# Kernel tuning notes

Measured on AMD Instinct MI355X. Metric: run time of the kernel, lower is better.

## Reference

```python
import jax, jax.numpy as jnp
import numpy as np

F_DIM = 256
N_HEADS = 4
D_Q = F_DIM // N_HEADS  # 64
EPS = 1e-6


def layer_norm(x, g, b):
    mu = jnp.mean(x, axis=-1, keepdims=True)
    var = jnp.mean(jnp.square(x - mu), axis=-1, keepdims=True)
    return (x - mu) * jax.lax.rsqrt(var + EPS) * g + b


def linear(x, W, b):
    # torch nn.Linear: y = x @ W.T + b, W: [out, in]
    return jnp.einsum('...i,oi->...o', x, W) + b


def setup_inputs() -> dict:
    key = jax.random.key(0)
    ks = jax.random.split(key, 16)
    f = F_DIM
    inp = {
        'code_map': jax.random.normal(ks[0], (8, 512, f), jnp.float32),
        'texture_map': jax.random.normal(ks[1], (8, 512, f), jnp.float32),
        'Wq': jax.random.normal(ks[2], (N_HEADS * D_Q, f), jnp.float32) * 0.02,
        'bq': jnp.zeros((N_HEADS * D_Q,), jnp.float32),
        'Wk': jax.random.normal(ks[3], (N_HEADS * D_Q, f), jnp.float32) * 0.02,
        'bk': jnp.zeros((N_HEADS * D_Q,), jnp.float32),
        'Wv': jax.random.normal(ks[4], (N_HEADS * D_Q, f), jnp.float32) * 0.02,
        'bv': jnp.zeros((N_HEADS * D_Q,), jnp.float32),
        'Wo': jax.random.normal(ks[5], (f, N_HEADS * D_Q), jnp.float32) * 0.02,
        'bo': jnp.zeros((f,), jnp.float32),
        'ln1_g': jnp.ones((f,), jnp.float32), 'ln1_b': jnp.zeros((f,), jnp.float32),
        'ln2_g': jnp.ones((f,), jnp.float32), 'ln2_b': jnp.zeros((f,), jnp.float32),
        'ffln_g': jnp.ones((f,), jnp.float32), 'ffln_b': jnp.zeros((f,), jnp.float32),
        'W1': jax.random.normal(ks[6], (f, f), jnp.float32) * 0.02,
        'b1': jnp.zeros((f,), jnp.float32),
        'W2': jax.random.normal(ks[7], (f, f), jnp.float32) * 0.02,
        'b2': jnp.zeros((f,), jnp.float32),
    }
    return inp


def reference(code_map, texture_map, Wq, bq, Wk, bk, Wv, bv, Wo, bo,
              ln1_g, ln1_b, ln2_g, ln2_b, ffln_g, ffln_b, W1, b1, W2, b2):
    n_code, V, f = code_map.shape
    bs = texture_map.shape[0]
    h, dq = N_HEADS, D_Q

    # LayerNorms (code side -> ln1, texture side -> ln2); expansion via repeat
    # is a pure broadcast, so keep code side [n_code,...] and texture side [bs,...].
    code2 = layer_norm(code_map, ln1_g, ln1_b)       # [n, V, f]
    tex2 = layer_norm(texture_map, ln2_g, ln2_b)     # [b, V, f]

    q = linear(tex2, Wq, bq).reshape(bs, V, h, dq)    # [b, V, h, d]
    k = linear(code2, Wk, bk).reshape(n_code, V, h, dq)
    v = linear(code2, Wv, bv).reshape(n_code, V, h, dq)

    scale = 1.0 / jnp.sqrt(jnp.asarray(dq, q.dtype))
    # scores: [b, n, h, Vq, Vk]
    scores = jnp.einsum('bqhd,nkhd->bnhqk', q, k) * scale
    attn = jax.nn.softmax(scores, axis=-1)
    ctx = jnp.einsum('bnhqk,nkhd->bnhqd', attn, v)    # [b, n, h, V, d]
    ctx = ctx.transpose(0, 1, 3, 2, 4).reshape(bs, n_code, V, h * dq)
    feat = linear(ctx, Wo, bo)                        # [b, n, V, f]

    x = texture_map[:, None, :, :] + feat             # residual with broadcast
    # ffR: MLP_res_block
    y = layer_norm(x, ffln_g, ffln_b)
    y = linear(jax.nn.relu(linear(y, W1, b1)), W2, b2)
    return x + y
```

## Files before the change

### kernel.cpp

```cpp
#include <hip/hip_runtime.h>
#include <hip/hip_bf16.h>

#define F 256
#define V 512
#define NB 8
#define NC 8
#define NH 4
#define DQ 64
#define EPS 1e-6f

typedef __hip_bfloat16 bf16;
typedef __attribute__((ext_vector_type(8))) short short8;
typedef __attribute__((ext_vector_type(4))) float f32x4;
typedef __attribute__((ext_vector_type(4))) unsigned uint4v;

__device__ __forceinline__ float b2f(bf16 x){ return __bfloat162float(x); }
__device__ __forceinline__ float shf(short s){
    return __bfloat162float(__builtin_bit_cast(bf16, (unsigned short)s));
}

#define MFMA(a,b,c) __builtin_amdgcn_mfma_f32_16x16x32_bf16((a),(b),(c),0,0,0)

__device__ __forceinline__ unsigned pack2bf(float a, float b){
    unsigned short ua = __builtin_bit_cast(unsigned short, __float2bfloat16(a));
    unsigned short ub = __builtin_bit_cast(unsigned short, __float2bfloat16(b));
    return (unsigned)ua | ((unsigned)ub << 16);
}

__global__ __launch_bounds__(256) void pre_kernel(const float* __restrict__ code,
                          const float* __restrict__ tex,
                          const float* __restrict__ ln1_g, const float* __restrict__ ln1_b,
                          const float* __restrict__ ln2_g, const float* __restrict__ ln2_b,
                          const float* __restrict__ w0, const float* __restrict__ w1,
                          const float* __restrict__ w2, const float* __restrict__ w3,
                          const float* __restrict__ w4, const float* __restrict__ w5,
                          bf16* __restrict__ cn, bf16* __restrict__ tn, bf16* __restrict__ tb,
                          bf16* __restrict__ wdst){
    if (blockIdx.x >= 2048){
        int bid = blockIdx.x - 2048;
        int which = bid >> 6;
        int idx = (((bid & 63) << 8) | threadIdx.x) << 2;
        const float* s = which==0?w0: which==1?w1: which==2?w2: which==3?w3: which==4?w4: w5;
        float4 v = *(const float4*)(s + idx);
        uint2 p; p.x = pack2bf(v.x, v.y); p.y = pack2bf(v.z, v.w);
        *(uint2*)(wdst + which * (F*F) + idx) = p;
        return;
    }
    int w = threadIdx.x >> 6, lane = threadIdx.x & 63;
    int r = blockIdx.x * 4 + w;
    int is_tex = r >> 12;
    int row = r & 4095;
    const float* src = is_tex ? tex : code;
    const float* g   = is_tex ? ln2_g : ln1_g;
    const float* be  = is_tex ? ln2_b : ln1_b;
    bf16* dst        = is_tex ? tn : cn;

    float4 x = *(const float4*)(src + row * F + lane * 4);
    if (is_tex){
        uint2 p; p.x = pack2bf(x.x, x.y); p.y = pack2bf(x.z, x.w);
        *(uint2*)(tb + row * F + lane * 4) = p;
    }
    float s = x.x + x.y + x.z + x.w;
    #pragma unroll
    for(int m = 1; m < 64; m <<= 1) s += __shfl_xor(s, m);
    float mu = s * (1.0f / F);
    float d0 = x.x - mu, d1 = x.y - mu, d2 = x.z - mu, d3 = x.w - mu;
    float q = d0*d0 + d1*d1 + d2*d2 + d3*d3;
    #pragma unroll
    for(int m = 1; m < 64; m <<= 1) q += __shfl_xor(q, m);
    float rs = rsqrtf(q * (1.0f / F) + EPS);
    float4 gg = *(const float4*)(g + lane * 4);
    float4 bb = *(const float4*)(be + lane * 4);
    uint2 p;
    p.x = pack2bf(d0 * rs * gg.x + bb.x, d1 * rs * gg.y + bb.y);
    p.y = pack2bf(d2 * rs * gg.z + bb.z, d3 * rs * gg.w + bb.w);
    *(uint2*)(dst + row * F + lane * 4) = p;
}

__global__ __launch_bounds__(256)
void qkv_kernel(const bf16* __restrict__ cn,
                const bf16* __restrict__ tn,
                const bf16* __restrict__ wbf,
                const float* __restrict__ bq,
                const float* __restrict__ bk,
                const float* __restrict__ bv,
                bf16* __restrict__ qn,
                bf16* __restrict__ k4,
                bf16* __restrict__ v4){
    __shared__ bf16 ts[64][72];
    int which = blockIdx.z;
    const bf16* in   = (which == 0) ? tn : cn;
    const bf16* wb   = wbf + which * (F * F);
    const float* bias = (which == 0) ? bq : (which == 1) ? bk : bv;

    int tid = threadIdx.x;
    int w = tid >> 6, lane = tid & 63;
    int lg = lane >> 4, li = lane & 15;
    int rowbase = blockIdx.x * 64 + w * 16;
    int colbase = blockIdx.y * 64;

    f32x4 acc[4];
    #pragma unroll
    for(int ni = 0; ni < 4; ni++) acc[ni] = (f32x4){0.f,0.f,0.f,0.f};

    const bf16* arow = in + (rowbase + li) * F + lg * 8;
    const bf16* brow = wb + (colbase + li) * F + lg * 8;

    #pragma unroll
    for(int kc = 0; kc < 8; kc++){
        short8 a = *(const short8*)(arow + kc * 32);
        #pragma unroll
        for(int ni = 0; ni < 4; ni++){
            short8 bbf = *(const short8*)(brow + ni * 16 * F + kc * 32);
            acc[ni] = MFMA(a, bbf, acc[ni]);
        }
    }

    if (which < 2){
        #pragma unroll
        for(int ni = 0; ni < 4; ni++)
            #pragma unroll
            for(int r = 0; r < 4; r++)
                ts[w * 16 + lg * 4 + r][ni * 16 + li] =
                    __float2bfloat16(acc[ni][r] + bias[colbase + ni * 16 + li]);
    } else {
        #pragma unroll
        for(int ni = 0; ni < 4; ni++)
            #pragma unroll
            for(int r = 0; r < 4; r++)
                ts[ni * 16 + li][w * 16 + lg * 4 + r] =
                    __float2bfloat16(acc[ni][r] + bias[colbase + ni * 16 + li]);
    }
    __syncthreads();

    if (which == 0){
        int rr = tid >> 2, gg2 = tid & 3;
        *(short8*)(qn + (blockIdx.x * 64 + rr) * F + colbase + gg2 * 16)
            = *(const short8*)&ts[rr][gg2 * 16];
    } else if (which == 1){
        int n = blockIdx.x >> 3;
        int kc2base = (blockIdx.x & 7) * 2;
        int hh = blockIdx.y;
        #pragma unroll
        for(int rep = 0; rep < 2; rep++){
            int c = tid + 256 * rep;
            int f = c >> 6, wf = c & 63;
            int lgp = wf >> 4, lip = wf & 15;
            int kc2l = f >> 2, kt = (f >> 1) & 1, ks = f & 1;
            int fi = ((n * 16 + kc2base + kc2l) * 2 + kt) * 8 + hh * 2 + ks;
            *(short8*)(k4 + fi * 512 + lgp * 128 + lip * 8)
                = *(const short8*)&ts[kc2l * 32 + kt * 16 + lip][ks * 32 + lgp * 8];
        }
    } else {
        int col = tid & 63, half = tid >> 6;
        int keybase = blockIdx.x * 64;
        int n = keybase >> 9;
        int keyl = (keybase & (V - 1)) + half * 16;
        int chunk = keyl >> 5, off = keyl & 31;
        *(short8*)(v4 + ((n * 16 + chunk) * F + colbase + col) * 32 + off)
            = *(const short8*)&ts[col][half * 16];
    }
}

__global__ __launch_bounds__(512, 4) void attn_mlp_kernel(const bf16* __restrict__ qn,
                                                          const bf16* __restrict__ k4,
                                                          const bf16* __restrict__ v4,
                                                          const bf16* __restrict__ wbf,
                                                          const float* __restrict__ bo,
                                                          const bf16* __restrict__ tb,
                                                          const float* __restrict__ ffg,
                                                          const float* __restrict__ ffb,
                                                          const float* __restrict__ b1,
                                                          const float* __restrict__ b2,
                                                          float* __restrict__ out){
    __shared__ bf16 xs[32][264];
    __shared__ float red[512], red2[512];
    __shared__ float stat[32][2];
    int n = blockIdx.x & 7, b = blockIdx.x >> 3, qt = blockIdx.y;
    int tid = threadIdx.x;
    int w = tid >> 6, lane = tid & 63;
    int h = w & 3, qh = w >> 2;
    int lg = lane >> 4, li = lane & 15;

    short8 qB[2];
    #pragma unroll
    for(int ks = 0; ks < 2; ks++)
        qB[ks] = *(const short8*)(qn + (b * V + qt * 32 + qh * 16 + li) * F
                                     + h * DQ + ks * 32 + lg * 8);

    f32x4 o[4];
    #pragma unroll
    for(int dt = 0; dt < 4; dt++) o[dt] = (f32x4){0.f,0.f,0.f,0.f};
    float l_acc = 0.f;

    const float scale = 0.125f;
    int g1 = lg & 1;
    int lhA = li | ((2 * g1) << 4);
    int lhB = lhA | 16;
    bool hi = lane >= 32;
    int fel = lg * 128 + li * 8;

    short8 kA0, kA1, kA2, kA3, vA0, vA1, vA2, vA3;
    {
        int fb = ((n * 16 + 0) * 2) * 8 + h * 2;
        kA0 = *(const short8*)(k4 + (fb + 0) * 512 + fel);
        kA1 = *(const short8*)(k4 + (fb + 1) * 512 + fel);
        kA2 = *(const short8*)(k4 + (fb + 8) * 512 + fel);
        kA3 = *(const short8*)(k4 + (fb + 9) * 512 + fel);
        const bf16* vb = v4 + ((n * 16 + 0) * F + h * DQ) * 32;
        vA0 = *(const short8*)(vb + (0 * 16 + li) * 32 + lg * 8);
        vA1 = *(const short8*)(vb + (1 * 16 + li) * 32 + lg * 8);
        vA2 = *(const short8*)(vb + (2 * 16 + li) * 32 + lg * 8);
        vA3 = *(const short8*)(vb + (3 * 16 + li) * 32 + lg * 8);
    }

    #pragma unroll
    for(int kc = 0; kc < 16; kc++){
        short8 nk0, nk1, nk2, nk3, nv0, nv1, nv2, nv3;
        if (kc < 15){
            int fb = ((n * 16 + kc + 1) * 2) * 8 + h * 2;
            nk0 = *(const short8*)(k4 + (fb + 0) * 512 + fel);
            nk1 = *(const short8*)(k4 + (fb + 1) * 512 + fel);
            nk2 = *(const short8*)(k4 + (fb + 8) * 512 + fel);
            nk3 = *(const short8*)(k4 + (fb + 9) * 512 + fel);
            const bf16* vb = v4 + ((n * 16 + kc + 1) * F + h * DQ) * 32;
            nv0 = *(const short8*)(vb + (0 * 16 + li) * 32 + lg * 8);
            nv1 = *(const short8*)(vb + (1 * 16 + li) * 32 + lg * 8);
            nv2 = *(const short8*)(vb + (2 * 16 + li) * 32 + lg * 8);
            nv3 = *(const short8*)(vb + (3 * 16 + li) * 32 + lg * 8);
        }

        f32x4 st0 = (f32x4){0.f,0.f,0.f,0.f};
        f32x4 st1 = (f32x4){0.f,0.f,0.f,0.f};
        __builtin_amdgcn_s_setprio(1);
        st0 = MFMA(kA0, qB[0], st0);
        st1 = MFMA(kA2, qB[0], st1);
        st0 = MFMA(kA1, qB[1], st0);
        st1 = MFMA(kA3, qB[1], st1);
        __builtin_amdgcn_s_setprio(0);

        float p[2][4], rsum = 0.f;
        #pragma unroll
        for(int r = 0; r < 4; r++){
            p[0][r] = __expf(st0[r] * scale);
            p[1][r] = __expf(st1[r] * scale);
            rsum += p[0][r] + p[1][r];
        }
        l_acc += rsum;

        unsigned pk00 = pack2bf(p[0][0], p[0][1]);
        unsigned pk01 = pack2bf(p[0][2], p[0][3]);
        unsigned pk10 = pack2bf(p[1][0], p[1][1]);
        unsigned pk11 = pack2bf(p[1][2], p[1][3]);

        unsigned d0a = __shfl((int)pk00, lhA, 64);
        unsigned d0b = __shfl((int)pk10, lhA, 64);
        unsigned d1a = __shfl((int)pk01, lhA, 64);
        unsigned d1b = __shfl((int)pk11, lhA, 64);
        unsigned d2a = __shfl((int)pk00, lhB, 64);
        unsigned d2b = __shfl((int)pk10, lhB, 64);
        unsigned d3a = __shfl((int)pk01, lhB, 64);
        unsigned d3b = __shfl((int)pk11, lhB, 64);
        uint4v uv;
        uv.x = hi ? d0b : d0a;
        uv.y = hi ? d1b : d1a;
        uv.z = hi ? d2b : d2a;
        uv.w = hi ? d3b : d3a;
        short8 pfrag = __builtin_bit_cast(short8, uv);

        __builtin_amdgcn_s_setprio(1);
        o[0] = MFMA(vA0, pfrag, o[0]);
        o[1] = MFMA(vA1, pfrag, o[1]);
        o[2] = MFMA(vA2, pfrag, o[2]);
        o[3] = MFMA(vA3, pfrag, o[3]);
        __builtin_amdgcn_s_setprio(0);

        kA0 = nk0; kA1 = nk1; kA2 = nk2; kA3 = nk3;
        vA0 = nv0; vA1 = nv1; vA2 = nv2; vA3 = nv3;
    }

    l_acc += __shfl_xor(l_acc, 16);
    l_acc += __shfl_xor(l_acc, 32);
    float inv = 1.0f / l_acc;

    #pragma unroll
    for(int dt = 0; dt < 4; dt++){
        uint2 pkd;
        pkd.x = pack2bf(o[dt][0] * inv, o[dt][1] * inv);
        pkd.y = pack2bf(o[dt][2] * inv, o[dt][3] * inv);
        *(uint2*)&xs[qh * 16 + li][h * DQ + dt * 16 + lg * 4] = pkd;
    }
    __syncthreads();

    const bf16* Wo = wbf + 3 * (F * F);
    int colbase = w * 32;
    f32x4 xac[2][2];
    #pragma unroll
    for(int mi = 0; mi < 2; mi++)
        #pragma unroll
        for(int ni = 0; ni < 2; ni++) xac[mi][ni] = (f32x4){0.f,0.f,0.f,0.f};
    #pragma unroll
    for(int kc = 0; kc < 8; kc++){
        short8 a0 = *(const short8*)&xs[li][kc * 32 + lg * 8];
        short8 a1 = *(const short8*)&xs[16 + li][kc * 32 + lg * 8];
        #pragma unroll
        for(int ni = 0; ni < 2; ni++){
            short8 bw = *(const short8*)(Wo + (colbase + ni * 16 + li) * F + kc * 32 + lg * 8);
            xac[0][ni] = MFMA(a0, bw, xac[0][ni]);
            xac[1][ni] = MFMA(a1, bw, xac[1][ni]);
        }
    }
    float xres[2][2][4];
    #pragma unroll
    for(int mi = 0; mi < 2; mi++)
        #pragma unroll
        for(int r = 0; r < 4; r++){
            int qrel = mi * 16 + lg * 4 + r;
            #pragma unroll
            for(int ni = 0; ni < 2; ni++){
                int col = colbase + ni * 16 + li;
                xres[mi][ni][r] = xac[mi][ni][r] + bo[col]
                                + b2f(tb[(b * V + qt * 32 + qrel) * F + col]);
            }
        }
    __syncthreads();
    #pragma unroll
    for(int mi = 0; mi < 2; mi++)
        #pragma unroll
        for(int r = 0; r < 4; r++){
            int qrel = mi * 16 + lg * 4 + r;
            #pragma unroll
            for(int ni = 0; ni < 2; ni++)
                xs[qrel][colbase + ni * 16 + li] = __float2bfloat16(xres[mi][ni][r]);
        }
    __syncthreads();

    int row = tid >> 4, sub = tid & 15;
    short8 xa = *(const short8*)&xs[row][sub * 16];
    short8 xb2 = *(const short8*)&xs[row][sub * 16 + 8];
    float sum = 0.f, sq = 0.f;
    #pragma unroll
    for(int j = 0; j < 8; j++){
        float v0 = shf(xa[j]), v1 = shf(xb2[j]);
        sum += v0 + v1; sq += v0 * v0 + v1 * v1;
    }
    red[tid] = sum; red2[tid] = sq;
    __syncthreads();
    if (tid < 32){
        float s = 0.f, q2 = 0.f;
        #pragma unroll
        for(int i = 0; i < 16; i++){ s += red[tid * 16 + i]; q2 += red2[tid * 16 + i]; }
        float mu = s * (1.0f / F);
        float var = q2 * (1.0f / F) - mu * mu;
        stat[tid][0] = mu;
        stat[tid][1] = rsqrtf(var + EPS);
    }
    __syncthreads();
    {
        float mu = stat[row][0], rsv = stat[row][1];
        float nv[16];
        #pragma unroll
        for(int j = 0; j < 8; j++){
            int c0 = sub * 16 + j, c1 = sub * 16 + 8 + j;
            nv[j]     = (shf(xa[j])  - mu) * rsv * ffg[c0] + ffb[c0];
            nv[8 + j] = (shf(xb2[j]) - mu) * rsv * ffg[c1] + ffb[c1];
        }
        uint4v pa, pb;
        pa.x = pack2bf(nv[0], nv[1]);  pa.y = pack2bf(nv[2], nv[3]);
        pa.z = pack2bf(nv[4], nv[5]);  pa.w = pack2bf(nv[6], nv[7]);
        pb.x = pack2bf(nv[8], nv[9]);  pb.y = pack2bf(nv[10], nv[11]);
        pb.z = pack2bf(nv[12], nv[13]); pb.w = pack2bf(nv[14], nv[15]);
        *(short8*)&xs[row][sub * 16]     = __builtin_bit_cast(short8, pa);
        *(short8*)&xs[row][sub * 16 + 8] = __builtin_bit_cast(short8, pb);
    }
    __syncthreads();

    const bf16* W1b = wbf + 4 * (F * F);
    f32x4 hac[2][2];
    #pragma unroll
    for(int mi = 0; mi < 2; mi++)
        #pragma unroll
        for(int ni = 0; ni < 2; ni++) hac[mi][ni] = (f32x4){0.f,0.f,0.f,0.f};
    #pragma unroll
    for(int kc = 0; kc < 8; kc++){
        short8 a0 = *(const short8*)&xs[li][kc * 32 + lg * 8];
        short8 a1 = *(const short8*)&xs[16 + li][kc * 32 + lg * 8];
        #pragma unroll
        for(int ni = 0; ni < 2; ni++){
            short8 bw = *(const short8*)(W1b + (colbase + ni * 16 + li) * F + kc * 32 + lg * 8);
            hac[0][ni] = MFMA(a0, bw, hac[0][ni]);
            hac[1][ni] = MFMA(a1, bw, hac[1][ni]);
        }
    }
    __syncthreads();
    #pragma unroll
    for(int mi = 0; mi < 2; mi++)
        #pragma unroll
        for(int r = 0; r < 4; r++){
            int rr = mi * 16 + lg * 4 + r;
            #pragma unroll
            for(int ni = 0; ni < 2; ni++){
                int col = colbase + ni * 16 + li;
                xs[rr][col] = __float2bfloat16(fmaxf(hac[mi][ni][r] + b1[col], 0.f));
            }
        }
    __syncthreads();

    const bf16* W2b = wbf + 5 * (F * F);
    f32x4 oac[2][2];
    #pragma unroll
    for(int mi = 0; mi < 2; mi++)
        #pragma unroll
        for(int ni = 0; ni < 2; ni++) oac[mi][ni] = (f32x4){0.f,0.f,0.f,0.f};
    #pragma unroll
    for(int kc = 0; kc < 8; kc++){
        short8 a0 = *(const short8*)&xs[li][kc * 32 + lg * 8];
        short8 a1 = *(const short8*)&xs[16 + li][kc * 32 + lg * 8];
        #pragma unroll
        for(int ni = 0; ni < 2; ni++){
            short8 bw = *(const short8*)(W2b + (colbase + ni * 16 + li) * F + kc * 32 + lg * 8);
            oac[0][ni] = MFMA(a0, bw, oac[0][ni]);
            oac[1][ni] = MFMA(a1, bw, oac[1][ni]);
        }
    }
    #pragma unroll
    for(int mi = 0; mi < 2; mi++)
        #pragma unroll
        for(int r = 0; r < 4; r++){
            int qrel = mi * 16 + lg * 4 + r;
            int ro = (b * NC + n) * V + qt * 32 + qrel;
            #pragma unroll
            for(int ni = 0; ni < 2; ni++){
                int col = colbase + ni * 16 + li;
                out[ro * F + col] = oac[mi][ni][r] + b2[col] + xres[mi][ni][r];
            }
        }
}

extern "C" void kernel_launch(void* const* d_in, const int* in_sizes, int n_in,
                              void* d_out, int out_size, void* d_ws, size_t ws_size,
                              hipStream_t stream) {
    const float* code_map = (const float*)d_in[0];
    const float* tex_map  = (const float*)d_in[1];
    const float* Wq = (const float*)d_in[2];  const float* bq = (const float*)d_in[3];
    const float* Wk = (const float*)d_in[4];  const float* bk = (const float*)d_in[5];
    const float* Wv = (const float*)d_in[6];  const float* bv = (const float*)d_in[7];
    const float* Wo = (const float*)d_in[8];  const float* bo = (const float*)d_in[9];
    const float* ln1_g = (const float*)d_in[10]; const float* ln1_b = (const float*)d_in[11];
    const float* ln2_g = (const float*)d_in[12]; const float* ln2_b = (const float*)d_in[13];
    const float* ffln_g = (const float*)d_in[14]; const float* ffln_b = (const float*)d_in[15];
    const float* W1 = (const float*)d_in[16]; const float* b1 = (const float*)d_in[17];
    const float* W2 = (const float*)d_in[18]; const float* b2 = (const float*)d_in[19];
    float* out = (float*)d_out;

    bf16* ws  = (bf16*)d_ws;
    bf16* qn  = ws;
    bf16* k4  = qn + 1048576;
    bf16* v4  = k4 + 1048576;
    bf16* cn  = v4 + 1048576;
    bf16* tn  = cn + 1048576;
    bf16* tb  = tn + 1048576;
    bf16* wbf = tb + 1048576;

    pre_kernel<<<2048 + 384, 256, 0, stream>>>(code_map, tex_map, ln1_g, ln1_b, ln2_g, ln2_b,
                                               Wq, Wk, Wv, Wo, W1, W2, cn, tn, tb, wbf);
    qkv_kernel<<<dim3(64, 4, 3), 256, 0, stream>>>(cn, tn, wbf, bq, bk, bv, qn, k4, v4);
    attn_mlp_kernel<<<dim3(64, 16), 512, 0, stream>>>(qn, k4, v4, wbf, bo, tb,
                                                      ffln_g, ffln_b, b1, b2, out);
}
```

Before: 219.2 us.

## Double query rows per attention block to reuse K/V and weight fragments

Each block of the fused attention+MLP kernel now handles 64 query rows instead of 32. Each wave processes two 16-row query tiles, so every K/V fragment loaded from global memory feeds twice as many MFMAs, and Wo/W1/W2 fragments are reused across four row tiles. The grid is halved, the exp is switched to exp2f with a folded log2e scale, and the LayerNorm gamma/beta loads are vectorized. The cost is more accumulator registers and LDS per block, which may lower occupancy under the launch bounds, and fewer blocks to spread across CUs.

```diff
diff --git a/kernel.cpp b/kernel.cpp
--- a/kernel.cpp
+++ b/kernel.cpp
@@ -173,27 +173,31 @@
                                                           const float* __restrict__ b1,
                                                           const float* __restrict__ b2,
                                                           float* __restrict__ out){
-    __shared__ bf16 xs[32][264];
+    __shared__ bf16 xs[64][264];
     __shared__ float red[512], red2[512];
-    __shared__ float stat[32][2];
+    __shared__ float stat[64][2];
     int n = blockIdx.x & 7, b = blockIdx.x >> 3, qt = blockIdx.y;
     int tid = threadIdx.x;
     int w = tid >> 6, lane = tid & 63;
     int h = w & 3, qh = w >> 2;
     int lg = lane >> 4, li = lane & 15;
 
-    short8 qB[2];
-    #pragma unroll
-    for(int ks = 0; ks < 2; ks++)
-        qB[ks] = *(const short8*)(qn + (b * V + qt * 32 + qh * 16 + li) * F
-                                     + h * DQ + ks * 32 + lg * 8);
-
-    f32x4 o[4];
-    #pragma unroll
-    for(int dt = 0; dt < 4; dt++) o[dt] = (f32x4){0.f,0.f,0.f,0.f};
-    float l_acc = 0.f;
-
-    const float scale = 0.125f;
+    short8 qB[2][2];
+    #pragma unroll
+    for(int qq = 0; qq < 2; qq++)
+        #pragma unroll
+        for(int ks = 0; ks < 2; ks++)
+            qB[qq][ks] = *(const short8*)(qn + (b * V + qt * 64 + qh * 32 + qq * 16 + li) * F
+                                             + h * DQ + ks * 32 + lg * 8);
+
+    f32x4 o[2][4];
+    #pragma unroll
+    for(int qq = 0; qq < 2; qq++)
+        #pragma unroll
+        for(int dt = 0; dt < 4; dt++) o[qq][dt] = (f32x4){0.f,0.f,0.f,0.f};
+    float l_acc[2] = {0.f, 0.f};
+
+    const float cexp = 0.125f * 1.44269504088896f;
     int g1 = lg & 1;
     int lhA = li | ((2 * g1) << 4);
     int lhB = lhA | 16;
@@ -230,89 +234,114 @@
             nv3 = *(const short8*)(vb + (3 * 16 + li) * 32 + lg * 8);
         }
 
-        f32x4 st0 = (f32x4){0.f,0.f,0.f,0.f};
-        f32x4 st1 = (f32x4){0.f,0.f,0.f,0.f};
+        f32x4 st[2][2];
+        #pragma unroll
+        for(int qq = 0; qq < 2; qq++){
+            st[qq][0] = (f32x4){0.f,0.f,0.f,0.f};
+            st[qq][1] = (f32x4){0.f,0.f,0.f,0.f};
+        }
         __builtin_amdgcn_s_setprio(1);
-        st0 = MFMA(kA0, qB[0], st0);
-        st1 = MFMA(kA2, qB[0], st1);
-        st0 = MFMA(kA1, qB[1], st0);
-        st1 = MFMA(kA3, qB[1], st1);
+        st[0][0] = MFMA(kA0, qB[0][0], st[0][0]);
+        st[0][1] = MFMA(kA2, qB[0][0], st[0][1]);
+        st[1][0] = MFMA(kA0, qB[1][0], st[1][0]);
+        st[1][1] = MFMA(kA2, qB[1][0], st[1][1]);
+        st[0][0] = MFMA(kA1, qB[0][1], st[0][0]);
+        st[0][1] = MFMA(kA3, qB[0][1], st[0][1]);
+        st[1][0] = MFMA(kA1, qB[1][1], st[1][0]);
+        st[1][1] = MFMA(kA3, qB[1][1], st[1][1]);
         __builtin_amdgcn_s_setprio(0);
 
-        float p[2][4], rsum = 0.f;
-        #pragma unroll
-        for(int r = 0; r < 4; r++){
-            p[0][r] = __expf(st0[r] * scale);
-            p[1][r] = __expf(st1[r] * scale);
-            rsum += p[0][r] + p[1][r];
-        }
-        l_acc += rsum;
-
-        unsigned pk00 = pack2bf(p[0][0], p[0][1]);
-        unsigned pk01 = pack2bf(p[0][2], p[0][3]);
-        unsigned pk10 = pack2bf(p[1][0], p[1][1]);
-        unsigned pk11 = pack2bf(p[1][2], p[1][3]);
-
-        unsigned d0a = __shfl((int)pk00, lhA, 64);
-        unsigned d0b = __shfl((int)pk10, lhA, 64);
-        unsigned d1a = __shfl((int)pk01, lhA, 64);
-        unsigned d1b = __shfl((int)pk11, lhA, 64);
-        unsigned d2a = __shfl((int)pk00, lhB, 64);
-        unsigned d2b = __shfl((int)pk10, lhB, 64);
-        unsigned d3a = __shfl((int)pk01, lhB, 64);
-        unsigned d3b = __shfl((int)pk11, lhB, 64);
-        uint4v uv;
-        uv.x = hi ? d0b : d0a;
-        uv.y = hi ? d1b : d1a;
-        uv.z = hi ? d2b : d2a;
-        uv.w = hi ? d3b : d3a;
-        short8 pfrag = __builtin_bit_cast(short8, uv);
+        short8 pfrag[2];
+        #pragma unroll
+        for(int qq = 0; qq < 2; qq++){
+            float p0[4], p1[4], rsum = 0.f;
+            #pragma unroll
+            for(int r = 0; r < 4; r++){
+                p0[r] = exp2f(st[qq][0][r] * cexp);
+                p1[r] = exp2f(st[qq][1][r] * cexp);
+                rsum += p0[r] + p1[r];
+            }
+            l_acc[qq] += rsum;
+
+            unsigned pk00 = pack2bf(p0[0], p0[1]);
+            unsigned pk01 = pack2bf(p0[2], p0[3]);
+            unsigned pk10 = pack2bf(p1[0], p1[1]);
+            unsigned pk11 = pack2bf(p1[2], p1[3]);
+
+            unsigned d0a = __shfl((int)pk00, lhA, 64);
+            unsigned d0b = __shfl((int)pk10, lhA, 64);
+            unsigned d1a = __shfl((int)pk01, lhA, 64);
+            unsigned d1b = __shfl((int)pk11, lhA, 64);
+            unsigned d2a = __shfl((int)pk00, lhB, 64);
+            unsigned d2b = __shfl((int)pk10, lhB, 64);
+            unsigned d3a = __shfl((int)pk01, lhB, 64);
+            unsigned d3b = __shfl((int)pk11, lhB, 64);
+            uint4v uv;
+            uv.x = hi ? d0b : d0a;
+            uv.y = hi ? d1b : d1a;
+            uv.z = hi ? d2b : d2a;
+            uv.w = hi ? d3b : d3a;
+            pfrag[qq] = __builtin_bit_cast(short8, uv);
+        }
 
         __builtin_amdgcn_s_setprio(1);
-        o[0] = MFMA(vA0, pfrag, o[0]);
-        o[1] = MFMA(vA1, pfrag, o[1]);
-        o[2] = MFMA(vA2, pfrag, o[2]);
-        o[3] = MFMA(vA3, pfrag, o[3]);
+        o[0][0] = MFMA(vA0, pfrag[0], o[0][0]);
+        o[0][1] = MFMA(vA1, pfrag[0], o[0][1]);
+        o[0][2] = MFMA(vA2, pfrag[0], o[0][2]);
+        o[0][3] = MFMA(vA3, pfrag[0], o[0][3]);
+        o[1][0] = MFMA(vA0, pfrag[1], o[1][0]);
+        o[1][1] = MFMA(vA1, pfrag[1], o[1][1]);
+        o[1][2] = MFMA(vA2, pfrag[1], o[1][2]);
+        o[1][3] = MFMA(vA3, pfrag[1], o[1][3]);
         __builtin_amdgcn_s_setprio(0);
 
         kA0 = nk0; kA1 = nk1; kA2 = nk2; kA3 = nk3;
         vA0 = nv0; vA1 = nv1; vA2 = nv2; vA3 = nv3;
     }
 
-    l_acc += __shfl_xor(l_acc, 16);
-    l_acc += __shfl_xor(l_acc, 32);
-    float inv = 1.0f / l_acc;
-
-    #pragma unroll
-    for(int dt = 0; dt < 4; dt++){
-        uint2 pkd;
-        pkd.x = pack2bf(o[dt][0] * inv, o[dt][1] * inv);
-        pkd.y = pack2bf(o[dt][2] * inv, o[dt][3] * inv);
-        *(uint2*)&xs[qh * 16 + li][h * DQ + dt * 16 + lg * 4] = pkd;
-    }
+    float inv[2];
+    #pragma unroll
+    for(int qq = 0; qq < 2; qq++){
+        l_acc[qq] += __shfl_xor(l_acc[qq], 16);
+        l_acc[qq] += __shfl_xor(l_acc[qq], 32);
+        inv[qq] = 1.0f / l_acc[qq];
+    }
+
+    #pragma unroll
+    for(int qq = 0; qq < 2; qq++)
+        #pragma unroll
+        for(int dt = 0; dt < 4; dt++){
+            uint2 pkd;
+            pkd.x = pack2bf(o[qq][dt][0] * inv[qq], o[qq][dt][1] * inv[qq]);
+            pkd.y = pack2bf(o[qq][dt][2] * inv[qq], o[qq][dt][3] * inv[qq]);
+            *(uint2*)&xs[qh * 32 + qq * 16 + li][h * DQ + dt * 16 + lg * 4] = pkd;
+        }
     __syncthreads();
 
     const bf16* Wo = wbf + 3 * (F * F);
     int colbase = w * 32;
-    f32x4 xac[2][2];
-    #pragma unroll
-    for(int mi = 0; mi < 2; mi++)
+    f32x4 xac[4][2];
+    #pragma unroll
+    for(int mi = 0; mi < 4; mi++)
         #pragma unroll
         for(int ni = 0; ni < 2; ni++) xac[mi][ni] = (f32x4){0.f,0.f,0.f,0.f};
     #pragma unroll
     for(int kc = 0; kc < 8; kc++){
-        short8 a0 = *(const short8*)&xs[li][kc * 32 + lg * 8];
-        short8 a1 = *(const short8*)&xs[16 + li][kc * 32 + lg * 8];
+        short8 a[4];
+        #pragma unroll
+        for(int mi = 0; mi < 4; mi++)
+            a[mi] = *(const short8*)&xs[mi * 16 + li][kc * 32 + lg * 8];
         #pragma unroll
         for(int ni = 0; ni < 2; ni++){
             short8 bw = *(const short8*)(Wo + (colbase + ni * 16 + li) * F + kc * 32 + lg * 8);
-            xac[0][ni] = MFMA(a0, bw, xac[0][ni]);
-            xac[1][ni] = MFMA(a1, bw, xac[1][ni]);
-        }
-    }
-    float xres[2][2][4];
-    #pragma unroll
-    for(int mi = 0; mi < 2; mi++)
+            #pragma unroll
+            for(int mi = 0; mi < 4; mi++)
+                xac[mi][ni] = MFMA(a[mi], bw, xac[mi][ni]);
+        }
+    }
+    float xres[4][2][4];
+    #pragma unroll
+    for(int mi = 0; mi < 4; mi++)
         #pragma unroll
         for(int r = 0; r < 4; r++){
             int qrel = mi * 16 + lg * 4 + r;
@@ -320,12 +349,12 @@
             for(int ni = 0; ni < 2; ni++){
                 int col = colbase + ni * 16 + li;
                 xres[mi][ni][r] = xac[mi][ni][r] + bo[col]
-                                + b2f(tb[(b * V + qt * 32 + qrel) * F + col]);
+                                + b2f(tb[(b * V + qt * 64 + qrel) * F + col]);
             }
         }
     __syncthreads();
     #pragma unroll
-    for(int mi = 0; mi < 2; mi++)
+    for(int mi = 0; mi < 4; mi++)
         #pragma unroll
         for(int r = 0; r < 4; r++){
             int qrel = mi * 16 + lg * 4 + r;
@@ -335,21 +364,25 @@
         }
     __syncthreads();
 
-    int row = tid >> 4, sub = tid & 15;
-    short8 xa = *(const short8*)&xs[row][sub * 16];
-    short8 xb2 = *(const short8*)&xs[row][sub * 16 + 8];
+    int row = tid >> 3, sub = tid & 7;
+    short8 xv[4];
+    #pragma unroll
+    for(int seg = 0; seg < 4; seg++)
+        xv[seg] = *(const short8*)&xs[row][sub * 32 + seg * 8];
     float sum = 0.f, sq = 0.f;
     #pragma unroll
-    for(int j = 0; j < 8; j++){
-        float v0 = shf(xa[j]), v1 = shf(xb2[j]);
-        sum += v0 + v1; sq += v0 * v0 + v1 * v1;
-    }
+    for(int seg = 0; seg < 4; seg++)
+        #pragma unroll
+        for(int j = 0; j < 8; j++){
+            float v0 = shf(xv[seg][j]);
+            sum += v0; sq += v0 * v0;
+        }
     red[tid] = sum; red2[tid] = sq;
     __syncthreads();
-    if (tid < 32){
+    if (tid < 64){
         float s = 0.f, q2 = 0.f;
         #pragma unroll
-        for(int i = 0; i < 16; i++){ s += red[tid * 16 + i]; q2 += red2[tid * 16 + i]; }
+        for(int i = 0; i < 8; i++){ s += red[tid * 8 + i]; q2 += red2[tid * 8 + i]; }
         float mu = s * (1.0f / F);
         float var = q2 * (1.0f / F) - mu * mu;
         stat[tid][0] = mu;
@@ -358,43 +391,52 @@
     __syncthreads();
     {
         float mu = stat[row][0], rsv = stat[row][1];
-        float nv[16];
-        #pragma unroll
-        for(int j = 0; j < 8; j++){
-            int c0 = sub * 16 + j, c1 = sub * 16 + 8 + j;
-            nv[j]     = (shf(xa[j])  - mu) * rsv * ffg[c0] + ffb[c0];
-            nv[8 + j] = (shf(xb2[j]) - mu) * rsv * ffg[c1] + ffb[c1];
-        }
-        uint4v pa, pb;
-        pa.x = pack2bf(nv[0], nv[1]);  pa.y = pack2bf(nv[2], nv[3]);
-        pa.z = pack2bf(nv[4], nv[5]);  pa.w = pack2bf(nv[6], nv[7]);
-        pb.x = pack2bf(nv[8], nv[9]);  pb.y = pack2bf(nv[10], nv[11]);
-        pb.z = pack2bf(nv[12], nv[13]); pb.w = pack2bf(nv[14], nv[15]);
-        *(short8*)&xs[row][sub * 16]     = __builtin_bit_cast(short8, pa);
-        *(short8*)&xs[row][sub * 16 + 8] = __builtin_bit_cast(short8, pb);
+        #pragma unroll
+        for(int seg = 0; seg < 4; seg++){
+            int c = sub * 32 + seg * 8;
+            float4 g0 = *(const float4*)(ffg + c);
+            float4 g1 = *(const float4*)(ffg + c + 4);
+            float4 f0 = *(const float4*)(ffb + c);
+            float4 f1 = *(const float4*)(ffb + c + 4);
+            float n0 = (shf(xv[seg][0]) - mu) * rsv * g0.x + f0.x;
+            float n1 = (shf(xv[seg][1]) - mu) * rsv * g0.y + f0.y;
+            float n2 = (shf(xv[seg][2]) - mu) * rsv * g0.z + f0.z;
+            float n3 = (shf(xv[seg][3]) - mu) * rsv * g0.w + f0.w;
+            float n4 = (shf(xv[seg][4]) - mu) * rsv * g1.x + f1.x;
+            float n5 = (shf(xv[seg][5]) - mu) * rsv * g1.y + f1.y;
+            float n6 = (shf(xv[seg][6]) - mu) * rsv * g1.z + f1.z;
+            float n7 = (shf(xv[seg][7]) - mu) * rsv * g1.w + f1.w;
+            uint4v pk;
+            pk.x = pack2bf(n0, n1); pk.y = pack2bf(n2, n3);
+            pk.z = pack2bf(n4, n5); pk.w = pack2bf(n6, n7);
+            *(short8*)&xs[row][c] = __builtin_bit_cast(short8, pk);
+        }
     }
     __syncthreads();
 
     const bf16* W1b = wbf + 4 * (F * F);
-    f32x4 hac[2][2];
-    #pragma unroll
-    for(int mi = 0; mi < 2; mi++)
+    f32x4 hac[4][2];
+    #pragma unroll
+    for(int mi = 0; mi < 4; mi++)
         #pragma unroll
         for(int ni = 0; ni < 2; ni++) hac[mi][ni] = (f32x4){0.f,0.f,0.f,0.f};
     #pragma unroll
     for(int kc = 0; kc < 8; kc++){
-        short8 a0 = *(const short8*)&xs[li][kc * 32 + lg * 8];
-        short8 a1 = *(const short8*)&xs[16 + li][kc * 32 + lg * 8];
+        short8 a[4];
+        #pragma unroll
+        for(int mi = 0; mi < 4; mi++)
+            a[mi] = *(const short8*)&xs[mi * 16 + li][kc * 32 + lg * 8];
         #pragma unroll
         for(int ni = 0; ni < 2; ni++){
             short8 bw = *(const short8*)(W1b + (colbase + ni * 16 + li) * F + kc * 32 + lg * 8);
-            hac[0][ni] = MFMA(a0, bw, hac[0][ni]);
-            hac[1][ni] = MFMA(a1, bw, hac[1][ni]);
-        }
-    }
-    __syncthreads();
-    #pragma unroll
-    for(int mi = 0; mi < 2; mi++)
+            #pragma unroll
+            for(int mi = 0; mi < 4; mi++)
+                hac[mi][ni] = MFMA(a[mi], bw, hac[mi][ni]);
+        }
+    }
+    __syncthreads();
+    #pragma unroll
+    for(int mi = 0; mi < 4; mi++)
         #pragma unroll
         for(int r = 0; r < 4; r++){
             int rr = mi * 16 + lg * 4 + r;
@@ -407,28 +449,31 @@
     __syncthreads();
 
     const bf16* W2b = wbf + 5 * (F * F);
-    f32x4 oac[2][2];
-    #pragma unroll
-    for(int mi = 0; mi < 2; mi++)
+    f32x4 oac[4][2];
+    #pragma unroll
+    for(int mi = 0; mi < 4; mi++)
         #pragma unroll
         for(int ni = 0; ni < 2; ni++) oac[mi][ni] = (f32x4){0.f,0.f,0.f,0.f};
     #pragma unroll
     for(int kc = 0; kc < 8; kc++){
-        short8 a0 = *(const short8*)&xs[li][kc * 32 + lg * 8];
-        short8 a1 = *(const short8*)&xs[16 + li][kc * 32 + lg * 8];
+        short8 a[4];
+        #pragma unroll
+        for(int mi = 0; mi < 4; mi++)
+            a[mi] = *(const short8*)&xs[mi * 16 + li][kc * 32 + lg * 8];
         #pragma unroll
         for(int ni = 0; ni < 2; ni++){
             short8 bw = *(const short8*)(W2b + (colbase + ni * 16 + li) * F + kc * 32 + lg * 8);
-            oac[0][ni] = MFMA(a0, bw, oac[0][ni]);
-            oac[1][ni] = MFMA(a1, bw, oac[1][ni]);
-        }
-    }
-    #pragma unroll
-    for(int mi = 0; mi < 2; mi++)
+            #pragma unroll
+            for(int mi = 0; mi < 4; mi++)
+                oac[mi][ni] = MFMA(a[mi], bw, oac[mi][ni]);
+        }
+    }
+    #pragma unroll
+    for(int mi = 0; mi < 4; mi++)
         #pragma unroll
         for(int r = 0; r < 4; r++){
             int qrel = mi * 16 + lg * 4 + r;
-            int ro = (b * NC + n) * V + qt * 32 + qrel;
+            int ro = (b * NC + n) * V + qt * 64 + qrel;
             #pragma unroll
             for(int ni = 0; ni < 2; ni++){
                 int col = colbase + ni * 16 + li;
@@ -465,6 +510,6 @@
     pre_kernel<<<2048 + 384, 256, 0, stream>>>(code_map, tex_map, ln1_g, ln1_b, ln2_g, ln2_b,
                                                Wq, Wk, Wv, Wo, W1, W2, cn, tn, tb, wbf);
     qkv_kernel<<<dim3(64, 4, 3), 256, 0, stream>>>(cn, tn, wbf, bq, bk, bv, qn, k4, v4);
-    attn_mlp_kernel<<<dim3(64, 16), 512, 0, stream>>>(qn, k4, v4, wbf, bo, tb,
-                                                      ffln_g, ffln_b, b1, b2, out);
+    attn_mlp_kernel<<<dim3(64, 8), 512, 0, stream>>>(qn, k4, v4, wbf, bo, tb,
+                                                     ffln_g, ffln_b, b1, b2, out);
 }
```

After: 238.4 us. 8.8% more time.
